# Performance work log

Hardware: AMD Instinct MI355X
Metric: run time of the kernel (lower is better)

Reference implementation:

```python
import jax, jax.numpy as jnp
import numpy as np

B, S, D, H = 2, 2048, 1024, 16
HD = D // H  # head_dim = 64


def setup_inputs() -> dict:
    key = jax.random.key(0)
    ks = jax.random.split(key, 6)
    scale = 1.0 / np.sqrt(D)
    return {
        "x": jax.random.normal(ks[0], (B, S, D), dtype=jnp.float32),
        "Wq": jax.random.normal(ks[1], (D, D), dtype=jnp.float32) * scale,
        "bq": jnp.zeros((D,), dtype=jnp.float32),
        "Wk": jax.random.normal(ks[2], (D, D), dtype=jnp.float32) * scale,
        "bk": jnp.zeros((D,), dtype=jnp.float32),
        "Wv": jax.random.normal(ks[3], (D, D), dtype=jnp.float32) * scale,
        "bv": jnp.zeros((D,), dtype=jnp.float32),
        "Wo": jax.random.normal(ks[4], (D, D), dtype=jnp.float32) * scale,
        "bo": jnp.zeros((D,), dtype=jnp.float32),
    }


def reference(x, Wq, bq, Wk, bk, Wv, bv, Wo, bo):
    b, s, d = x.shape
    # q/k/v projections; torch Linear computes x @ W.T + b (W here stored as [out,in])
    q = (x @ Wq.T + bq).reshape(b, s, H, HD).transpose(0, 2, 1, 3)  # [b,h,s,hd]
    k = (x @ Wk.T + bk).reshape(b, s, H, HD).transpose(0, 2, 1, 3)
    v = (x @ Wv.T + bv).reshape(b, s, H, HD).transpose(0, 2, 1, 3)
    scores = jnp.einsum("bhqd,bhkd->bhqk", q, k) / jnp.sqrt(jnp.float32(HD))
    attn = jax.nn.softmax(scores, axis=-1)  # dropout p=0.0 -> identity
    ctx = jnp.einsum("bhqk,bhkd->bhqd", attn, v)
    ctx = ctx.transpose(0, 2, 1, 3).reshape(b, s, d)
    out = ctx @ Wo.T + bo
    return out, attn
```

## Files before the change

### kernel.cpp

```cpp
#include <hip/hip_runtime.h>
#include <hip/hip_bf16.h>


typedef __attribute__((ext_vector_type(8))) __bf16 bf16x8;
typedef __attribute__((ext_vector_type(8))) short short8;
typedef __attribute__((ext_vector_type(4))) float f32x4;
typedef __attribute__((ext_vector_type(4))) float float4v;
typedef __attribute__((ext_vector_type(4))) unsigned short ushort4v;
typedef __attribute__((ext_vector_type(8))) unsigned short ushort8v;

#define DEV static __device__ __forceinline__

DEV unsigned short f2bf(float f) {
  unsigned int u = __builtin_bit_cast(unsigned int, f);
  u += 0x7FFFu + ((u >> 16) & 1u);
  return (unsigned short)(u >> 16);
}

DEV f32x4 mfma16(short8 a, short8 b, f32x4 c) {
  return __builtin_amdgcn_mfma_f32_16x16x32_bf16(
      __builtin_bit_cast(bf16x8, a), __builtin_bit_cast(bf16x8, b), c, 0, 0, 0);
}

DEV void gld16(const void* g, void* l) {
  __builtin_amdgcn_global_load_lds(
      (const __attribute__((address_space(1))) void*)g,
      (__attribute__((address_space(3))) void*)l, 16, 0, 0);
}

__global__ __launch_bounds__(256) void cvt_all(
    const float* __restrict__ x, const float* __restrict__ wq,
    const float* __restrict__ wk, const float* __restrict__ wv,
    const float* __restrict__ wo, unsigned short* __restrict__ xb,
    unsigned short* __restrict__ wqb, unsigned short* __restrict__ wkb,
    unsigned short* __restrict__ wvb, unsigned short* __restrict__ wob) {
  const int bid = blockIdx.x;
  const float* s;
  unsigned short* d;
  int base;
  if (bid < 2048) {
    s = x; d = xb; base = bid * 2048;
  } else {
    const int j = bid - 2048, sel = j >> 9;
    s = sel == 0 ? wq : (sel == 1 ? wk : (sel == 2 ? wv : wo));
    d = sel == 0 ? wqb : (sel == 1 ? wkb : (sel == 2 ? wvb : wob));
    base = (j & 511) * 2048;
  }
  const int i = base + threadIdx.x * 8;
  float4v v0 = *(const float4v*)(s + i);
  float4v v1 = *(const float4v*)(s + i + 4);
  ushort8v o = {f2bf(v0[0]), f2bf(v0[1]), f2bf(v0[2]), f2bf(v0[3]),
                f2bf(v1[0]), f2bf(v1[1]), f2bf(v1[2]), f2bf(v1[3])};
  *(ushort8v*)(d + i) = o;
}

template <int WBF>
__global__ __launch_bounds__(256, 3) void gemm_qkv(
    const unsigned short* __restrict__ xb,
    const void* __restrict__ W0, const void* __restrict__ W1, const void* __restrict__ W2,
    const float* __restrict__ b0, const float* __restrict__ b1, const float* __restrict__ b2,
    unsigned short* __restrict__ Qw, unsigned short* __restrict__ Kw,
    unsigned short* __restrict__ Vt) {
  constexpr int K = 1024;
  __shared__ unsigned short As[2][128 * 32];
  __shared__ unsigned short Bs[2][128 * 32];
  const int tid = threadIdx.x, lane = tid & 63, w = tid >> 6;
  const int g = lane >> 4, ln = lane & 15;
  const int wm = (w >> 1) * 64, wn = (w & 1) * 64;
  const int work = ((int)blockIdx.x & 7) * 96 + ((int)blockIdx.x >> 3);
  const int t = work >> 8, tn = (work >> 5) & 7, tm = work & 31;
  const int m0 = tm * 128, n0 = tn * 128;
  const void* Wsel = t == 0 ? W0 : (t == 1 ? W1 : W2);
  const float* bsel = t == 0 ? b0 : (t == 1 ? b1 : b2);
  const float osc = t == 0 ? 0.125f : 1.0f;

  const unsigned short* Abase = xb + (size_t)(m0 + (tid >> 2)) * K + (tid & 3) * 8;
  const unsigned short* Bb16 = (const unsigned short*)Wsel + (size_t)(n0 + (tid >> 2)) * K + (tid & 3) * 8;
  const float* Bf32 = (const float*)Wsel + (size_t)(n0 + (tid >> 1)) * K + (tid & 1) * 16;
  const int bwoff = (tid >> 1) * 32 + (tid & 1) * 16;

  f32x4 acc[4][4] = {};

  gld16(Abase, &As[0][tid * 8]);
  gld16(Abase + (size_t)64 * K, &As[0][2048 + tid * 8]);
  if (WBF) {
    gld16(Bb16, &Bs[0][tid * 8]);
    gld16(Bb16 + (size_t)64 * K, &Bs[0][2048 + tid * 8]);
  } else {
    float4v u0 = *(const float4v*)Bf32, u1 = *(const float4v*)(Bf32 + 4);
    float4v u2 = *(const float4v*)(Bf32 + 8), u3 = *(const float4v*)(Bf32 + 12);
    ushort8v o0 = {f2bf(u0[0]), f2bf(u0[1]), f2bf(u0[2]), f2bf(u0[3]),
                   f2bf(u1[0]), f2bf(u1[1]), f2bf(u1[2]), f2bf(u1[3])};
    ushort8v o1 = {f2bf(u2[0]), f2bf(u2[1]), f2bf(u2[2]), f2bf(u2[3]),
                   f2bf(u3[0]), f2bf(u3[1]), f2bf(u3[2]), f2bf(u3[3])};
    *(ushort8v*)&Bs[0][bwoff] = o0;
    *(ushort8v*)&Bs[0][bwoff + 8] = o1;
  }

#pragma unroll 2
  for (int it = 0; it < 32; ++it) {
    __syncthreads();
    const int cur = it & 1, nxt = cur ^ 1;
    float4v u0, u1, u2, u3;
    if (it + 1 < 32) {
      const int k1 = (it + 1) * 32;
      gld16(Abase + k1, &As[nxt][tid * 8]);
      gld16(Abase + (size_t)64 * K + k1, &As[nxt][2048 + tid * 8]);
      if (WBF) {
        gld16(Bb16 + k1, &Bs[nxt][tid * 8]);
        gld16(Bb16 + (size_t)64 * K + k1, &Bs[nxt][2048 + tid * 8]);
      } else {
        u0 = *(const float4v*)(Bf32 + k1);
        u1 = *(const float4v*)(Bf32 + k1 + 4);
        u2 = *(const float4v*)(Bf32 + k1 + 8);
        u3 = *(const float4v*)(Bf32 + k1 + 12);
      }
    }
    short8 a[4], bfr[4];
#pragma unroll
    for (int fi = 0; fi < 4; ++fi)
      a[fi] = *(const short8*)&As[cur][(wm + fi * 16 + ln) * 32 + g * 8];
#pragma unroll
    for (int fj = 0; fj < 4; ++fj)
      bfr[fj] = *(const short8*)&Bs[cur][(wn + fj * 16 + ln) * 32 + g * 8];
#pragma unroll
    for (int fi = 0; fi < 4; ++fi)
#pragma unroll
      for (int fj = 0; fj < 4; ++fj) acc[fi][fj] = mfma16(a[fi], bfr[fj], acc[fi][fj]);
    if (!WBF && it + 1 < 32) {
      ushort8v o0 = {f2bf(u0[0]), f2bf(u0[1]), f2bf(u0[2]), f2bf(u0[3]),
                     f2bf(u1[0]), f2bf(u1[1]), f2bf(u1[2]), f2bf(u1[3])};
      ushort8v o1 = {f2bf(u2[0]), f2bf(u2[1]), f2bf(u2[2]), f2bf(u2[3]),
                     f2bf(u3[0]), f2bf(u3[1]), f2bf(u3[2]), f2bf(u3[3])};
      *(ushort8v*)&Bs[nxt][bwoff] = o0;
      *(ushort8v*)&Bs[nxt][bwoff + 8] = o1;
    }
  }

  if (t < 2) {
    unsigned short* Op = t == 0 ? Qw : Kw;
#pragma unroll
    for (int fi = 0; fi < 4; ++fi)
#pragma unroll
      for (int fj = 0; fj < 4; ++fj) {
        const int n = n0 + wn + fj * 16 + ln;
        const float bs = bsel[n];
#pragma unroll
        for (int rr = 0; rr < 4; ++rr) {
          const int m = m0 + wm + fi * 16 + 4 * g + rr;
          Op[(size_t)m * 1024 + n] = f2bf((acc[fi][fj][rr] + bs) * osc);
        }
      }
  } else {
    const int bb = m0 >> 11;
    const int s0 = (m0 & 2047) + wm;
#pragma unroll
    for (int fi = 0; fi < 4; ++fi)
#pragma unroll
      for (int fj = 0; fj < 4; ++fj) {
        const int n = n0 + wn + fj * 16 + ln;
        const float bs = bsel[n];
        ushort4v o = {f2bf(acc[fi][fj][0] + bs), f2bf(acc[fi][fj][1] + bs),
                      f2bf(acc[fi][fj][2] + bs), f2bf(acc[fi][fj][3] + bs)};
        *(ushort4v*)&Vt[(size_t)(bb * 1024 + n) * 2048 + s0 + fi * 16 + 4 * g] = o;
      }
  }
}

template <int WBF>
__global__ __launch_bounds__(256, 3) void gemm_o(const unsigned short* __restrict__ Cw,
                                                 const void* __restrict__ Wo,
                                                 const float* __restrict__ bo,
                                                 float* __restrict__ outp) {
  constexpr int K = 1024;
  __shared__ unsigned short As[2][128 * 32];
  __shared__ unsigned short Bs[2][64 * 32];
  const int tid = threadIdx.x, lane = tid & 63, w = tid >> 6;
  const int g = lane >> 4, ln = lane & 15;
  const int wm = (w >> 1) * 64, wn = (w & 1) * 32;
  const int work = ((int)blockIdx.x & 7) * 64 + ((int)blockIdx.x >> 3);
  const int m0 = (work & 31) * 128, n0 = (work >> 5) * 64;

  const unsigned short* Abase = Cw + (size_t)(m0 + (tid >> 2)) * K + (tid & 3) * 8;
  const unsigned short* Bb16 = (const unsigned short*)Wo + (size_t)(n0 + (tid >> 2)) * K + (tid & 3) * 8;
  const float* Bf32 = (const float*)Wo + (size_t)(n0 + (tid >> 2)) * K + (tid & 3) * 8;
  const int bwoff = (tid >> 2) * 32 + (tid & 3) * 8;

  f32x4 acc[4][2] = {};

  gld16(Abase, &As[0][tid * 8]);
  gld16(Abase + (size_t)64 * K, &As[0][2048 + tid * 8]);
  if (WBF) {
    gld16(Bb16, &Bs[0][tid * 8]);
  } else {
    float4v u0 = *(const float4v*)Bf32, u1 = *(const float4v*)(Bf32 + 4);
    ushort8v o = {f2bf(u0[0]), f2bf(u0[1]), f2bf(u0[2]), f2bf(u0[3]),
                  f2bf(u1[0]), f2bf(u1[1]), f2bf(u1[2]), f2bf(u1[3])};
    *(ushort8v*)&Bs[0][bwoff] = o;
  }

#pragma unroll 2
  for (int it = 0; it < 32; ++it) {
    __syncthreads();
    const int cur = it & 1, nxt = cur ^ 1;
    float4v u0, u1;
    if (it + 1 < 32) {
      const int k1 = (it + 1) * 32;
      gld16(Abase + k1, &As[nxt][tid * 8]);
      gld16(Abase + (size_t)64 * K + k1, &As[nxt][2048 + tid * 8]);
      if (WBF) {
        gld16(Bb16 + k1, &Bs[nxt][tid * 8]);
      } else {
        u0 = *(const float4v*)(Bf32 + k1);
        u1 = *(const float4v*)(Bf32 + k1 + 4);
      }
    }
    short8 a[4], bfr[2];
#pragma unroll
    for (int fi = 0; fi < 4; ++fi)
      a[fi] = *(const short8*)&As[cur][(wm + fi * 16 + ln) * 32 + g * 8];
#pragma unroll
    for (int fj = 0; fj < 2; ++fj)
      bfr[fj] = *(const short8*)&Bs[cur][(wn + fj * 16 + ln) * 32 + g * 8];
#pragma unroll
    for (int fi = 0; fi < 4; ++fi)
#pragma unroll
      for (int fj = 0; fj < 2; ++fj) acc[fi][fj] = mfma16(a[fi], bfr[fj], acc[fi][fj]);
    if (!WBF && it + 1 < 32) {
      ushort8v o = {f2bf(u0[0]), f2bf(u0[1]), f2bf(u0[2]), f2bf(u0[3]),
                    f2bf(u1[0]), f2bf(u1[1]), f2bf(u1[2]), f2bf(u1[3])};
      *(ushort8v*)&Bs[nxt][bwoff] = o;
    }
  }

#pragma unroll
  for (int fi = 0; fi < 4; ++fi)
#pragma unroll
    for (int fj = 0; fj < 2; ++fj) {
      const int n = n0 + wn + fj * 16 + ln;
      const float bs = bo[n];
#pragma unroll
      for (int rr = 0; rr < 4; ++rr) {
        const int m = m0 + wm + fi * 16 + 4 * g + rr;
        outp[(size_t)m * 1024 + n] = acc[fi][fj][rr] + bs;
      }
    }
}

__global__ __launch_bounds__(512, 4) void attn_kernel(
    const unsigned short* __restrict__ Qg, const unsigned short* __restrict__ Kg,
    const unsigned short* __restrict__ Vt, float* __restrict__ attn_out,
    unsigned short* __restrict__ ctx) {
  constexpr int LDP = 72;
  __shared__ unsigned short Ps[128 * LDP];
  __shared__ unsigned short Ks[2][64 * 64];
  __shared__ unsigned short Vs[2][64 * 64];
  const int tid = threadIdx.x, lane = tid & 63, w = tid >> 6;
  const int g = lane >> 4, ln = lane & 15;
  const int work = ((int)blockIdx.x & 7) * 64 + ((int)blockIdx.x >> 3);
  const int qt = work & 15, h = (work >> 4) & 15, b = work >> 8;
  const int q0 = qt * 128;
  const size_t kbase = (size_t)b * 2048 * 1024 + (size_t)h * 64;
  const size_t vbase = ((size_t)b * 1024 + h * 64) * 2048;

  for (int cidx = tid; cidx < 1024; cidx += 512) {
    const int r = cidx >> 3, c = (cidx & 7) * 8;
    *(ushort8v*)&Ps[r * LDP + c] =
        *(const ushort8v*)(Qg + kbase + (size_t)(q0 + r) * 1024 + c);
  }
  const int sr = tid >> 3, sb = tid & 7;
  const int swz = ((sb ^ (sr & 7)) * 8);
  const unsigned short* Ksrc = Kg + kbase + (size_t)sr * 1024 + swz;
  const unsigned short* Vsrc = Vt + vbase + (size_t)sr * 2048 + swz;
  __syncthreads();

  short8 qf[2];
#pragma unroll
  for (int hh = 0; hh < 2; ++hh)
    qf[hh] = *(const short8*)&Ps[(w * 16 + ln) * LDP + hh * 32 + 8 * g];

  float lp = 0.f;
  gld16(Ksrc, &Ks[0][tid * 8]);
#pragma unroll 2
  for (int kc = 0; kc < 32; ++kc) {
    __syncthreads();
    if (kc + 1 < 32)
      gld16(Ksrc + (size_t)(kc + 1) * 64 * 1024, &Ks[(kc + 1) & 1][tid * 8]);
    const unsigned short* Kc = Ks[kc & 1];
#pragma unroll
    for (int fk = 0; fk < 4; ++fk) {
      const int row = fk * 16 + ln;
      const short8 kf0 = *(const short8*)&Kc[row * 64 + ((g ^ (ln & 7)) * 8)];
      const short8 kf1 = *(const short8*)&Kc[row * 64 + (((4 + g) ^ (ln & 7)) * 8)];
      f32x4 z = {0.f, 0.f, 0.f, 0.f};
      z = mfma16(kf0, qf[0], z);
      z = mfma16(kf1, qf[1], z);
      lp += __expf(z[0]) + __expf(z[1]) + __expf(z[2]) + __expf(z[3]);
    }
  }
  lp += __shfl_xor(lp, 16);
  lp += __shfl_xor(lp, 32);
  const float linv = 1.f / lp;

  __syncthreads();
  gld16(Ksrc, &Ks[0][tid * 8]);
  gld16(Vsrc, &Vs[0][tid * 8]);
  f32x4 c_[4] = {};
  const size_t attnbase = ((size_t)(b * 16 + h) * 2048 + q0 + w * 16) * 2048;
#pragma unroll 2
  for (int kc = 0; kc < 32; ++kc) {
    __syncthreads();
    if (kc + 1 < 32) {
      gld16(Ksrc + (size_t)(kc + 1) * 64 * 1024, &Ks[(kc + 1) & 1][tid * 8]);
      gld16(Vsrc + (kc + 1) * 64, &Vs[(kc + 1) & 1][tid * 8]);
    }
    const unsigned short* Kc = Ks[kc & 1];
    const unsigned short* Vc = Vs[kc & 1];
#pragma unroll
    for (int fk = 0; fk < 4; ++fk) {
      const int row = fk * 16 + ln;
      const short8 kf0 = *(const short8*)&Kc[row * 64 + ((g ^ (ln & 7)) * 8)];
      const short8 kf1 = *(const short8*)&Kc[row * 64 + (((4 + g) ^ (ln & 7)) * 8)];
      f32x4 z = {0.f, 0.f, 0.f, 0.f};
      z = mfma16(kf0, qf[0], z);
      z = mfma16(kf1, qf[1], z);
      float4v pv = {__expf(z[0]) * linv, __expf(z[1]) * linv, __expf(z[2]) * linv,
                    __expf(z[3]) * linv};
      *(float4v*)&attn_out[attnbase + (size_t)ln * 2048 + kc * 64 + fk * 16 + 4 * g] = pv;
      ushort4v pb = {f2bf(pv[0]), f2bf(pv[1]), f2bf(pv[2]), f2bf(pv[3])};
      *(ushort4v*)&Ps[(w * 16 + ln) * LDP + fk * 16 + 4 * g] = pb;
    }
#pragma unroll
    for (int ks = 0; ks < 2; ++ks) {
      const short8 pa = *(const short8*)&Ps[(w * 16 + ln) * LDP + ks * 32 + 8 * g];
#pragma unroll
      for (int fd = 0; fd < 4; ++fd) {
        const int d = fd * 16 + ln;
        const short8 vb = *(const short8*)&Vc[d * 64 + (((ks * 4 + g) ^ (ln & 7)) * 8)];
        c_[fd] = mfma16(pa, vb, c_[fd]);
      }
    }
  }

#pragma unroll
  for (int fd = 0; fd < 4; ++fd)
#pragma unroll
    for (int rr = 0; rr < 4; ++rr) {
      const int q = w * 16 + 4 * g + rr;
      ctx[(size_t)(b * 2048 + q0 + q) * 1024 + h * 64 + fd * 16 + ln] = f2bf(c_[fd][rr]);
    }
}

extern "C" void kernel_launch(void* const* d_in, const int* in_sizes, int n_in,
                              void* d_out, int out_size, void* d_ws, size_t ws_size,
                              hipStream_t stream) {
  const float* x  = (const float*)d_in[0];
  const float* Wq = (const float*)d_in[1];
  const float* bq = (const float*)d_in[2];
  const float* Wk = (const float*)d_in[3];
  const float* bk = (const float*)d_in[4];
  const float* Wv = (const float*)d_in[5];
  const float* bv = (const float*)d_in[6];
  const float* Wo = (const float*)d_in[7];
  const float* bo = (const float*)d_in[8];

  float* outp = (float*)d_out;
  float* attnp = outp + (size_t)4194304;

  unsigned short* Qw = (unsigned short*)d_ws;
  unsigned short* Kw = Qw + (size_t)4194304;
  unsigned short* Vt = Kw + (size_t)4194304;
  unsigned short* Cw = Vt + (size_t)4194304;

  const bool wbf = ws_size >= (size_t)40 * 1024 * 1024;
  dim3 blk(256, 1, 1);

  if (wbf) {
    unsigned short* Wqb = Cw + (size_t)4194304;
    unsigned short* Wkb = Wqb + (size_t)1048576;
    unsigned short* Wvb = Wkb + (size_t)1048576;
    unsigned short* Wob = Wvb + (size_t)1048576;
    cvt_all<<<dim3(4096), blk, 0, stream>>>(x, Wq, Wk, Wv, Wo, Cw, Wqb, Wkb, Wvb, Wob);
    gemm_qkv<1><<<dim3(768), blk, 0, stream>>>(Cw, Wqb, Wkb, Wvb, bq, bk, bv, Qw, Kw, Vt);
    attn_kernel<<<dim3(512), dim3(512), 0, stream>>>(Qw, Kw, Vt, attnp, Cw);
    gemm_o<1><<<dim3(512), blk, 0, stream>>>(Cw, Wob, bo, outp);
  } else {
    cvt_all<<<dim3(2048), blk, 0, stream>>>(x, Wq, Wk, Wv, Wo, Cw, nullptr, nullptr,
                                            nullptr, nullptr);
    gemm_qkv<0><<<dim3(768), blk, 0, stream>>>(Cw, Wq, Wk, Wv, bq, bk, bv, Qw, Kw, Vt);
    attn_kernel<<<dim3(512), dim3(512), 0, stream>>>(Qw, Kw, Vt, attnp, Cw);
    gemm_o<0><<<dim3(512), blk, 0, stream>>>(Cw, Wo, bo, outp);
  }
}
```

Measured before the change: 251.9 us.

## Use exp2 with folded log2e scale, enlarge O-proj tiles, add MFMA priority hints

The Q scale now folds log2(e) into 1/sqrt(64), so the attention kernel can call the hardware exp2 instruction instead of __expf. The output projection GEMM moves from 128x64 to 128x128 tiles with 256 blocks, which raises data reuse per block but halves the block count. s_setprio hints are placed around the MFMA sequences in attention to favour matrix issue across waves. The larger tile needs more registers and LDS, which may lower occupancy, and 256 blocks may leave compute units underfilled.

```diff
diff --git a/kernel.cpp b/kernel.cpp
--- a/kernel.cpp
+++ b/kernel.cpp
@@ -17,6 +17,14 @@
   return (unsigned short)(u >> 16);
 }
 
+DEV float exp2v(float x) {
+#if __has_builtin(__builtin_amdgcn_exp2f)
+  return __builtin_amdgcn_exp2f(x);
+#else
+  return exp2f(x);
+#endif
+}
+
 DEV f32x4 mfma16(short8 a, short8 b, f32x4 c) {
   return __builtin_amdgcn_mfma_f32_16x16x32_bf16(
       __builtin_bit_cast(bf16x8, a), __builtin_bit_cast(bf16x8, b), c, 0, 0, 0);
@@ -27,6 +35,8 @@
       (const __attribute__((address_space(1))) void*)g,
       (__attribute__((address_space(3))) void*)l, 16, 0, 0);
 }
+
+#define QSCALE 0.18033688011112042f
 
 __global__ __launch_bounds__(256) void cvt_all(
     const float* __restrict__ x, const float* __restrict__ wq,
@@ -72,7 +82,7 @@
   const int m0 = tm * 128, n0 = tn * 128;
   const void* Wsel = t == 0 ? W0 : (t == 1 ? W1 : W2);
   const float* bsel = t == 0 ? b0 : (t == 1 ? b1 : b2);
-  const float osc = t == 0 ? 0.125f : 1.0f;
+  const float osc = t == 0 ? QSCALE : 1.0f;
 
   const unsigned short* Abase = xb + (size_t)(m0 + (tid >> 2)) * K + (tid & 3) * 8;
   const unsigned short* Bb16 = (const unsigned short*)Wsel + (size_t)(n0 + (tid >> 2)) * K + (tid & 3) * 8;
@@ -174,69 +184,80 @@
                                                  float* __restrict__ outp) {
   constexpr int K = 1024;
   __shared__ unsigned short As[2][128 * 32];
-  __shared__ unsigned short Bs[2][64 * 32];
+  __shared__ unsigned short Bs[2][128 * 32];
   const int tid = threadIdx.x, lane = tid & 63, w = tid >> 6;
   const int g = lane >> 4, ln = lane & 15;
-  const int wm = (w >> 1) * 64, wn = (w & 1) * 32;
-  const int work = ((int)blockIdx.x & 7) * 64 + ((int)blockIdx.x >> 3);
-  const int m0 = (work & 31) * 128, n0 = (work >> 5) * 64;
+  const int wm = (w >> 1) * 64, wn = (w & 1) * 64;
+  const int work = ((int)blockIdx.x & 7) * 32 + ((int)blockIdx.x >> 3);
+  const int m0 = (work & 31) * 128, n0 = (work >> 5) * 128;
 
   const unsigned short* Abase = Cw + (size_t)(m0 + (tid >> 2)) * K + (tid & 3) * 8;
   const unsigned short* Bb16 = (const unsigned short*)Wo + (size_t)(n0 + (tid >> 2)) * K + (tid & 3) * 8;
-  const float* Bf32 = (const float*)Wo + (size_t)(n0 + (tid >> 2)) * K + (tid & 3) * 8;
-  const int bwoff = (tid >> 2) * 32 + (tid & 3) * 8;
-
-  f32x4 acc[4][2] = {};
+  const float* Bf32 = (const float*)Wo + (size_t)(n0 + (tid >> 1)) * K + (tid & 1) * 16;
+  const int bwoff = (tid >> 1) * 32 + (tid & 1) * 16;
+
+  f32x4 acc[4][4] = {};
 
   gld16(Abase, &As[0][tid * 8]);
   gld16(Abase + (size_t)64 * K, &As[0][2048 + tid * 8]);
   if (WBF) {
     gld16(Bb16, &Bs[0][tid * 8]);
+    gld16(Bb16 + (size_t)64 * K, &Bs[0][2048 + tid * 8]);
   } else {
     float4v u0 = *(const float4v*)Bf32, u1 = *(const float4v*)(Bf32 + 4);
-    ushort8v o = {f2bf(u0[0]), f2bf(u0[1]), f2bf(u0[2]), f2bf(u0[3]),
-                  f2bf(u1[0]), f2bf(u1[1]), f2bf(u1[2]), f2bf(u1[3])};
-    *(ushort8v*)&Bs[0][bwoff] = o;
+    float4v u2 = *(const float4v*)(Bf32 + 8), u3 = *(const float4v*)(Bf32 + 12);
+    ushort8v o0 = {f2bf(u0[0]), f2bf(u0[1]), f2bf(u0[2]), f2bf(u0[3]),
+                   f2bf(u1[0]), f2bf(u1[1]), f2bf(u1[2]), f2bf(u1[3])};
+    ushort8v o1 = {f2bf(u2[0]), f2bf(u2[1]), f2bf(u2[2]), f2bf(u2[3]),
+                   f2bf(u3[0]), f2bf(u3[1]), f2bf(u3[2]), f2bf(u3[3])};
+    *(ushort8v*)&Bs[0][bwoff] = o0;
+    *(ushort8v*)&Bs[0][bwoff + 8] = o1;
   }
 
 #pragma unroll 2
   for (int it = 0; it < 32; ++it) {
     __syncthreads();
     const int cur = it & 1, nxt = cur ^ 1;
-    float4v u0, u1;
+    float4v u0, u1, u2, u3;
     if (it + 1 < 32) {
       const int k1 = (it + 1) * 32;
       gld16(Abase + k1, &As[nxt][tid * 8]);
       gld16(Abase + (size_t)64 * K + k1, &As[nxt][2048 + tid * 8]);
       if (WBF) {
         gld16(Bb16 + k1, &Bs[nxt][tid * 8]);
+        gld16(Bb16 + (size_t)64 * K + k1, &Bs[nxt][2048 + tid * 8]);
       } else {
         u0 = *(const float4v*)(Bf32 + k1);
         u1 = *(const float4v*)(Bf32 + k1 + 4);
-      }
-    }
-    short8 a[4], bfr[2];
+        u2 = *(const float4v*)(Bf32 + k1 + 8);
+        u3 = *(const float4v*)(Bf32 + k1 + 12);
+      }
+    }
+    short8 a[4], bfr[4];
 #pragma unroll
     for (int fi = 0; fi < 4; ++fi)
       a[fi] = *(const short8*)&As[cur][(wm + fi * 16 + ln) * 32 + g * 8];
 #pragma unroll
-    for (int fj = 0; fj < 2; ++fj)
+    for (int fj = 0; fj < 4; ++fj)
       bfr[fj] = *(const short8*)&Bs[cur][(wn + fj * 16 + ln) * 32 + g * 8];
 #pragma unroll
     for (int fi = 0; fi < 4; ++fi)
 #pragma unroll
-      for (int fj = 0; fj < 2; ++fj) acc[fi][fj] = mfma16(a[fi], bfr[fj], acc[fi][fj]);
+      for (int fj = 0; fj < 4; ++fj) acc[fi][fj] = mfma16(a[fi], bfr[fj], acc[fi][fj]);
     if (!WBF && it + 1 < 32) {
-      ushort8v o = {f2bf(u0[0]), f2bf(u0[1]), f2bf(u0[2]), f2bf(u0[3]),
-                    f2bf(u1[0]), f2bf(u1[1]), f2bf(u1[2]), f2bf(u1[3])};
-      *(ushort8v*)&Bs[nxt][bwoff] = o;
+      ushort8v o0 = {f2bf(u0[0]), f2bf(u0[1]), f2bf(u0[2]), f2bf(u0[3]),
+                     f2bf(u1[0]), f2bf(u1[1]), f2bf(u1[2]), f2bf(u1[3])};
+      ushort8v o1 = {f2bf(u2[0]), f2bf(u2[1]), f2bf(u2[2]), f2bf(u2[3]),
+                     f2bf(u3[0]), f2bf(u3[1]), f2bf(u3[2]), f2bf(u3[3])};
+      *(ushort8v*)&Bs[nxt][bwoff] = o0;
+      *(ushort8v*)&Bs[nxt][bwoff + 8] = o1;
     }
   }
 
 #pragma unroll
   for (int fi = 0; fi < 4; ++fi)
 #pragma unroll
-    for (int fj = 0; fj < 2; ++fj) {
+    for (int fj = 0; fj < 4; ++fj) {
       const int n = n0 + wn + fj * 16 + ln;
       const float bs = bo[n];
 #pragma unroll
@@ -293,9 +314,11 @@
       const short8 kf0 = *(const short8*)&Kc[row * 64 + ((g ^ (ln & 7)) * 8)];
       const short8 kf1 = *(const short8*)&Kc[row * 64 + (((4 + g) ^ (ln & 7)) * 8)];
       f32x4 z = {0.f, 0.f, 0.f, 0.f};
+      __builtin_amdgcn_s_setprio(1);
       z = mfma16(kf0, qf[0], z);
       z = mfma16(kf1, qf[1], z);
-      lp += __expf(z[0]) + __expf(z[1]) + __expf(z[2]) + __expf(z[3]);
+      __builtin_amdgcn_s_setprio(0);
+      lp += exp2v(z[0]) + exp2v(z[1]) + exp2v(z[2]) + exp2v(z[3]);
     }
   }
   lp += __shfl_xor(lp, 16);
@@ -322,10 +345,12 @@
       const short8 kf0 = *(const short8*)&Kc[row * 64 + ((g ^ (ln & 7)) * 8)];
       const short8 kf1 = *(const short8*)&Kc[row * 64 + (((4 + g) ^ (ln & 7)) * 8)];
       f32x4 z = {0.f, 0.f, 0.f, 0.f};
+      __builtin_amdgcn_s_setprio(1);
       z = mfma16(kf0, qf[0], z);
       z = mfma16(kf1, qf[1], z);
-      float4v pv = {__expf(z[0]) * linv, __expf(z[1]) * linv, __expf(z[2]) * linv,
-                    __expf(z[3]) * linv};
+      __builtin_amdgcn_s_setprio(0);
+      float4v pv = {exp2v(z[0]) * linv, exp2v(z[1]) * linv, exp2v(z[2]) * linv,
+                    exp2v(z[3]) * linv};
       *(float4v*)&attn_out[attnbase + (size_t)ln * 2048 + kc * 64 + fk * 16 + 4 * g] = pv;
       ushort4v pb = {f2bf(pv[0]), f2bf(pv[1]), f2bf(pv[2]), f2bf(pv[3])};
       *(ushort4v*)&Ps[(w * 16 + ln) * LDP + fk * 16 + 4 * g] = pb;
@@ -333,12 +358,14 @@
 #pragma unroll
     for (int ks = 0; ks < 2; ++ks) {
       const short8 pa = *(const short8*)&Ps[(w * 16 + ln) * LDP + ks * 32 + 8 * g];
+      __builtin_amdgcn_s_setprio(1);
 #pragma unroll
       for (int fd = 0; fd < 4; ++fd) {
         const int d = fd * 16 + ln;
         const short8 vb = *(const short8*)&Vc[d * 64 + (((ks * 4 + g) ^ (ln & 7)) * 8)];
         c_[fd] = mfma16(pa, vb, c_[fd]);
       }
+      __builtin_amdgcn_s_setprio(0);
     }
   }
 
@@ -383,12 +410,12 @@
     cvt_all<<<dim3(4096), blk, 0, stream>>>(x, Wq, Wk, Wv, Wo, Cw, Wqb, Wkb, Wvb, Wob);
     gemm_qkv<1><<<dim3(768), blk, 0, stream>>>(Cw, Wqb, Wkb, Wvb, bq, bk, bv, Qw, Kw, Vt);
     attn_kernel<<<dim3(512), dim3(512), 0, stream>>>(Qw, Kw, Vt, attnp, Cw);
-    gemm_o<1><<<dim3(512), blk, 0, stream>>>(Cw, Wob, bo, outp);
+    gemm_o<1><<<dim3(256), blk, 0, stream>>>(Cw, Wob, bo, outp);
   } else {
     cvt_all<<<dim3(2048), blk, 0, stream>>>(x, Wq, Wk, Wv, Wo, Cw, nullptr, nullptr,
                                             nullptr, nullptr);
     gemm_qkv<0><<<dim3(768), blk, 0, stream>>>(Cw, Wq, Wk, Wv, bq, bk, bv, Qw, Kw, Vt);
     attn_kernel<<<dim3(512), dim3(512), 0, stream>>>(Qw, Kw, Vt, attnp, Cw);
-    gemm_o<0><<<dim3(512), blk, 0, stream>>>(Cw, Wo, bo, outp);
-  }
-}
+    gemm_o<0><<<dim3(256), blk, 0, stream>>>(Cw, Wo, bo, outp);
+  }
+}
```

New measurement: 245.2 us. 1.03x faster.
